# Kernel optimization log

Hardware: AMD Instinct MI355X
Metric: run time of the kernel (lower is better)

The kernel has to match this reference:

```python
import jax, jax.numpy as jnp
import numpy as np

# Dimensions: E experts, T tokens, K hidden, I intermediate (gate+up fused -> 2I)
E, T, K, I = 8, 4096, 2048, 768
TOP_K = 2


def setup_inputs() -> dict:
    key = jax.random.key(0)
    ks = jax.random.split(key, 6)
    hidden_states = jax.random.normal(ks[0], (T, K), dtype=jnp.float32)
    router_logits = jax.random.normal(ks[1], (T, E), dtype=jnp.float32)
    # 2-bit codes {0,1,2} <-> ternary {-1,0,+1} (pack_i2s_weights maps w+1)
    w13_q = jax.random.randint(ks[2], (E, 2 * I, K), 0, 3, dtype=jnp.int32)
    w2_q = jax.random.randint(ks[3], (E, K, I), 0, 3, dtype=jnp.int32)
    # per-input-column alpha scales (always positive, realistic magnitude)
    alpha13 = jax.random.uniform(ks[4], (E, K), dtype=jnp.float32) * 0.04 + 0.01
    alpha2 = jax.random.uniform(ks[5], (E, I), dtype=jnp.float32) * 0.04 + 0.01
    return {
        "hidden_states": hidden_states,
        "router_logits": router_logits,
        "w13_q": w13_q,
        "w2_q": w2_q,
        "alpha13": alpha13,
        "alpha2": alpha2,
    }


def reference(hidden_states, router_logits, w13_q, w2_q, alpha13, alpha2):
    # --- routing: softmax + top-k + renormalize ---
    probs = jax.nn.softmax(router_logits, axis=-1)              # [T, E]
    topk_w, topk_ids = jax.lax.top_k(probs, TOP_K)              # [T, k]
    topk_w = topk_w / jnp.sum(topk_w, axis=-1, keepdims=True)
    # dense combine weights [T, E]; zero for unselected experts
    gates = jnp.sum(
        jax.nn.one_hot(topk_ids, E, dtype=topk_w.dtype) * topk_w[..., None],
        axis=1,
    )

    # --- dequant ternary weights: W = (code - 1) * alpha[input_col] ---
    W13 = (w13_q.astype(jnp.float32) - 1.0) * alpha13[:, None, :]  # [E, 2I, K]
    W2 = (w2_q.astype(jnp.float32) - 1.0) * alpha2[:, None, :]     # [E, K, I]

    # --- grouped expert GEMMs (x @ W^T per expert) ---
    h = jnp.einsum("tk,enk->etn", hidden_states, W13)            # [E, T, 2I]
    g, u = jnp.split(h, 2, axis=-1)
    a = jax.nn.silu(g) * u                                       # [E, T, I]
    y = jnp.einsum("eti,eni->etn", a, W2)                        # [E, T, K]

    # --- combine with routing weights ---
    out = jnp.einsum("te,etk->tk", gates, y)                     # [T, K]
    return out
```

## Files before the change

kernel.cpp:

```cpp
#include <hip/hip_runtime.h>
#include <math.h>

#define E_ 8
#define T_ 4096
#define K_ 2048
#define I_ 768
#define TWOI 1536
#define NPAIR (2*T_)

typedef unsigned short u16;
typedef signed char i8;
typedef __attribute__((ext_vector_type(8))) __bf16 bf16x8;
typedef __attribute__((ext_vector_type(4))) float f32x4;
typedef __attribute__((ext_vector_type(4))) int i32x4;
typedef __attribute__((ext_vector_type(4))) unsigned u32x4;
typedef __attribute__((ext_vector_type(8))) u16 u16x8;
typedef __attribute__((ext_vector_type(4))) u16 u16x4;
typedef __attribute__((ext_vector_type(4))) int int4v;
typedef __attribute__((ext_vector_type(4))) float float4v;

typedef __attribute__((address_space(3))) char lds_c;
typedef __attribute__((address_space(1))) const char g_c;

__device__ inline void gld16(const void* g, void* l) {
    __builtin_amdgcn_global_load_lds((g_c*)g, (lds_c*)l, 16, 0, 0);
}

__device__ inline u16 f2bf(float x) {
    unsigned u = __builtin_bit_cast(unsigned, x);
    unsigned r = 0x7fffu + ((u >> 16) & 1u);
    u += r;
    return (u16)(u >> 16);
}
__device__ inline float bf2f(u16 b) {
    unsigned u = ((unsigned)b) << 16;
    return __builtin_bit_cast(float, u);
}
__device__ inline unsigned pack4(int4v q) {
    return (unsigned)((unsigned char)(char)(q[0] - 1))
         | ((unsigned)((unsigned char)(char)(q[1] - 1)) << 8)
         | ((unsigned)((unsigned char)(char)(q[2] - 1)) << 16)
         | ((unsigned)((unsigned char)(char)(q[3] - 1)) << 24);
}

#define NBLK 2048
__global__ __launch_bounds__(256) void k_fusedA(
    const int* __restrict__ w13q, const int* __restrict__ w2q,
    const float* __restrict__ alpha2, const float* __restrict__ logits,
    const float* __restrict__ x, const float* __restrict__ alpha13,
    i8* __restrict__ wc13, u16* __restrict__ wb2,
    i8* __restrict__ xq, float* __restrict__ sx,
    int* __restrict__ tid2, float* __restrict__ tw, int* __restrict__ cursors)
{
    int tid = threadIdx.x;
    int bid = blockIdx.x;
    if (bid == 0 && tid < E_) cursors[tid] = 0;

    {
        const int4v* src = (const int4v*)w13q;
        unsigned* dst = (unsigned*)wc13;
        const long n = 6291456;
        const long stride = (long)NBLK * 256;
#pragma unroll 2
        for (long u = (long)bid * 256 + tid; u < n; u += stride) {
            int4v q = __builtin_nontemporal_load(src + u);
            dst[u] = pack4(q);
        }
    }
    {
        const int4v* src = (const int4v*)w2q;
        const long n = 3145728;
        const long stride = (long)NBLK * 256;
#pragma unroll 2
        for (long u = (long)bid * 256 + tid; u < n; u += stride) {
            long g = u * 4;
            int i = (int)(g % I_);
            int e = (int)(g / ((long)K_ * I_));
            int4v q = __builtin_nontemporal_load(src + u);
            float4v a = *(const float4v*)(alpha2 + e * I_ + i);
            u16x4 r;
            r[0] = f2bf((float)(q[0] - 1) * a[0]);
            r[1] = f2bf((float)(q[1] - 1) * a[1]);
            r[2] = f2bf((float)(q[2] - 1) * a[2]);
            r[3] = f2bf((float)(q[3] - 1) * a[3]);
            *(u16x4*)(wb2 + g) = r;
        }
    }
    {
        int wv = bid * 4 + (tid >> 6);
        if (wv < T_) {
            int lane = tid & 63;
            int t = wv;
            float l[E_];
#pragma unroll
            for (int e = 0; e < E_; ++e) l[e] = logits[t * E_ + e];
            int e0 = 0; float mx0 = l[0];
#pragma unroll
            for (int e = 1; e < E_; ++e) if (l[e] > mx0) { mx0 = l[e]; e0 = e; }
            int e1 = -1; float mx1 = -1e30f;
#pragma unroll
            for (int e = 0; e < E_; ++e) if (e != e0 && l[e] > mx1) { mx1 = l[e]; e1 = e; }

            float4v xr[8];
#pragma unroll
            for (int c = 0; c < 8; ++c)
                xr[c] = *(const float4v*)(x + (long)t * K_ + c * 256 + lane * 4);

#pragma unroll
            for (int s = 0; s < 2; ++s) {
                int e = s ? e1 : e0;
                int p = 2 * t + s;
                float4v xa[8];
                float m = 0.f;
#pragma unroll
                for (int c = 0; c < 8; ++c) {
                    float4v a = *(const float4v*)(alpha13 + (long)e * K_ + c * 256 + lane * 4);
                    xa[c] = xr[c] * a;
#pragma unroll
                    for (int j = 0; j < 4; ++j) m = fmaxf(m, fabsf(xa[c][j]));
                }
#pragma unroll
                for (int off = 32; off >= 1; off >>= 1) m = fmaxf(m, __shfl_xor(m, off));
                float inv = (m > 0.f) ? 127.0f / m : 0.f;
#pragma unroll
                for (int c = 0; c < 8; ++c) {
                    unsigned pk = 0;
#pragma unroll
                    for (int j = 0; j < 4; ++j) {
                        int qv = __float2int_rn(xa[c][j] * inv);
                        pk |= ((unsigned)(unsigned char)(char)qv) << (8 * j);
                    }
                    *(unsigned*)(xq + (long)p * K_ + c * 256 + lane * 4) = pk;
                }
                if (lane == 0) sx[p] = m / 127.0f;
            }
            if (lane == 0) {
                tid2[2 * t + 0] = e0; tid2[2 * t + 1] = e1;
                float w0 = 1.0f / (1.0f + expf(mx1 - mx0));
                tw[2 * t + 0] = w0; tw[2 * t + 1] = 1.0f - w0;
            }
        }
    }
}

__global__ __launch_bounds__(256) void k_lists2(
    const int* __restrict__ tid2, int* __restrict__ offsets,
    int* __restrict__ cursors, int* __restrict__ pairTok)
{
    int tid = threadIdx.x;
    int c[E_];
#pragma unroll
    for (int e = 0; e < E_; ++e) c[e] = 0;
    for (int j = 0; j < 32; ++j) {
        int v = tid2[tid * 32 + j];
#pragma unroll
        for (int e = 0; e < E_; ++e) c[e] += (v == e) ? 1 : 0;
    }
#pragma unroll
    for (int e = 0; e < E_; ++e)
#pragma unroll
        for (int off = 32; off >= 1; off >>= 1)
            c[e] += __shfl_xor(c[e], off);
    __shared__ int ws[4][E_];
    __shared__ int offs[E_ + 1];
    if ((tid & 63) == 0)
#pragma unroll
        for (int e = 0; e < E_; ++e) ws[tid >> 6][e] = c[e];
    __syncthreads();
    if (tid == 0) {
        int s2 = 0;
        for (int e = 0; e < E_; ++e) {
            int ce = ws[0][e] + ws[1][e] + ws[2][e] + ws[3][e];
            offs[e] = s2; s2 += ce;
        }
        offs[E_] = s2;
        if (blockIdx.x == 0)
            for (int e = 0; e <= E_; ++e) offsets[e] = offs[e];
    }
    __syncthreads();
    int t = blockIdx.x * 256 + tid;
#pragma unroll
    for (int s = 0; s < 2; ++s) {
        int e = tid2[t * 2 + s];
        int pos = atomicAdd(&cursors[e], 1);
        pairTok[offs[e] + pos] = (t << 1) | s;
    }
}

__global__ __launch_bounds__(512, 2) void k_g1i8(
    const i8* __restrict__ A,
    const i8* __restrict__ B,
    const int* __restrict__ pairTok, const int* __restrict__ offsets,
    const float* __restrict__ sx,
    u16* __restrict__ C)
{
    int bid = blockIdx.x;
    int e  = bid & 7;
    int r_ = bid >> 3;
    int mc = r_ / 6;
    int nch = r_ % 6;
    int base = offsets[e];
    int cnt  = offsets[e + 1] - base;
    int m0 = mc * 256;
    if (m0 >= cnt) return;
    int n0 = nch * 128;

    __shared__ __attribute__((aligned(16))) i8 SHM[131072];
    i8* As = SHM;
    i8* Bs = SHM + 65536;

    int tid = threadIdx.x;
    int lane = tid & 63;
    int wid = tid >> 6;
    int wr = wid >> 2, wc = wid & 3;
    int l15 = lane & 15;

    const i8* srcA[4];
    const i8* srcB[4];
#pragma unroll
    for (int j = 0; j < 4; ++j) {
        int chunk = j * 512 + tid;
        int row = chunk >> 3, ch = chunk & 7;
        int colsw = (ch ^ (row & 7)) * 16;
        int ra = m0 + row; if (ra >= cnt) ra = cnt - 1;
        srcA[j] = A + (long)pairTok[base + ra] * K_ + colsw;
        int grow = e * TWOI + (row >> 7) * I_ + n0 + (row & 127);
        srcB[j] = B + (long)grow * K_ + colsw;
    }

    auto stage = [&](int bs, int t) {
        int k0 = t * 128;
        i8* dA = As + bs * 32768;
        i8* dB = Bs + bs * 32768;
#pragma unroll
        for (int j = 0; j < 4; ++j) {
            gld16(srcA[j] + k0, dA + j * 8192 + tid * 16);
            gld16(srcB[j] + k0, dB + j * 8192 + tid * 16);
        }
    };

    int kq16 = ((lane >> 4) & 3) * 16;

    i32x4 a[4][2], b[4][2];
    i32x4 acc[8][4];
#pragma unroll
    for (int mf = 0; mf < 8; ++mf)
#pragma unroll
        for (int nf = 0; nf < 4; ++nf)
            acc[mf][nf] = (i32x4){0, 0, 0, 0};

    auto rdA = [&](int bs, int h64) {
#pragma unroll
        for (int mf = 0; mf < 4; ++mf) {
            int row = wr * 128 + h64 + mf * 16 + l15;
            const i8* p = As + bs * 32768 + row * 128;
            int xr = (row & 7) << 4;
            a[mf][0] = *(const i32x4*)(p + ((kq16) ^ xr));
            a[mf][1] = *(const i32x4*)(p + ((64 + kq16) ^ xr));
        }
    };
    auto rdB = [&](int bs) {
#pragma unroll
        for (int nf = 0; nf < 4; ++nf) {
            int row = wc * 64 + nf * 16 + l15;
            const i8* p = Bs + bs * 32768 + row * 128;
            int xr = (row & 7) << 4;
            b[nf][0] = *(const i32x4*)(p + ((kq16) ^ xr));
            b[nf][1] = *(const i32x4*)(p + ((64 + kq16) ^ xr));
        }
    };
    auto mm = [&](int mh) {
#pragma unroll
        for (int ks = 0; ks < 2; ++ks)
#pragma unroll
            for (int mf = 0; mf < 4; ++mf)
#pragma unroll
                for (int nf = 0; nf < 4; ++nf)
                    acc[mh * 4 + mf][nf] = __builtin_amdgcn_mfma_i32_16x16x64_i8(
                        a[mf][ks], b[nf][ks], acc[mh * 4 + mf][nf], 0, 0, 0);
    };
    auto compute = [&](int bs) {
        rdB(bs);
        rdA(bs, 0);
        mm(0);
        rdA(bs, 64);
        mm(1);
    };

    stage(0, 0);
    __syncthreads();
#pragma unroll 1
    for (int t = 0; t < 16; t += 2) {
        stage(1, t + 1);
        compute(0);
        __syncthreads();
        if (t + 2 < 16) stage(0, t + 2);
        compute(1);
        __syncthreads();
    }

    u16* flat = (u16*)SHM;
#pragma unroll
    for (int mf = 0; mf < 8; ++mf)
#pragma unroll
        for (int nf = 0; nf < 4; ++nf)
#pragma unroll
            for (int rg = 0; rg < 4; ++rg) {
                int row = wr * 128 + mf * 16 + (lane >> 4) * 4 + rg;
                int col = wc * 64 + nf * 16 + l15;
                flat[row * 256 + (col ^ ((row & 7) << 3))] = f2bf((float)acc[mf][nf][rg]);
            }
    __syncthreads();
    int row = tid >> 1;
    if (m0 + row < cnt) {
        float s = sx[pairTok[base + m0 + row]];
        int xr = (row & 7) << 3;
        int half = tid & 1;
        u16* dst = C + (long)(base + m0 + row) * I_ + n0 + half * 64;
#pragma unroll
        for (int jj = 0; jj < 8; ++jj) {
            u16x8 gv = *(const u16x8*)&flat[row * 256 + ((half * 64 + jj * 8) ^ xr)];
            u16x8 uv = *(const u16x8*)&flat[row * 256 + ((128 + half * 64 + jj * 8) ^ xr)];
            u16x8 r;
#pragma unroll
            for (int q = 0; q < 8; ++q) {
                float g = bf2f(gv[q]) * s, u = bf2f(uv[q]) * s;
                r[q] = f2bf(g / (1.0f + expf(-g)) * u);
            }
            *(u16x8*)(dst + jj * 8) = r;
        }
    }
}

__global__ __launch_bounds__(512, 2) void k_g2(
    const u16* __restrict__ A,
    const u16* __restrict__ B,
    const int* __restrict__ pairTok, const int* __restrict__ offsets,
    u16* __restrict__ C)
{
    int bid = blockIdx.x;
    int e  = bid & 7;
    int r_ = bid >> 3;
    int mc = r_ >> 3;
    int nch = r_ & 7;
    int base = offsets[e];
    int cnt  = offsets[e + 1] - base;
    int m0 = mc * 256;
    if (m0 >= cnt) return;
    int n0 = nch * 256;

    __shared__ __attribute__((aligned(16))) char SHM[131072];
    u16* ldsA = (u16*)SHM;
    u16* ldsB = (u16*)(SHM + 65536);

    int tid = threadIdx.x;
    int lane = tid & 63;
    int wid = tid >> 6;
    int wr = wid >> 2, wc = wid & 3;
    int l15 = lane & 15;

    const u16* srcA[2][2];
    const u16* srcB[2][2];
#pragma unroll
    for (int h = 0; h < 2; ++h)
#pragma unroll
        for (int j = 0; j < 2; ++j) {
            int slot = j * 512 + tid;
            int row = slot >> 3, ch = slot & 7;
            int colsw = (ch ^ (row & 7)) * 8;
            int ra = m0 + h * 128 + row;
            if (ra >= cnt) ra = cnt - 1;
            srcA[h][j] = A + (long)(base + ra) * I_ + colsw;
            long brow = (long)e * K_ + n0 + h * 128 + row;
            srcB[h][j] = B + brow * (long)I_ + colsw;
        }
    int d0 = tid * 8, d1 = (512 + tid) * 8;

    auto stage = [&](int bs, int t) {
        int k0 = t * 64;
        u16* dA = ldsA + bs * 16384;
        u16* dB = ldsB + bs * 16384;
#pragma unroll
        for (int h = 0; h < 2; ++h) {
            gld16(srcA[h][0] + k0, dA + h * 8192 + d0);
            gld16(srcA[h][1] + k0, dA + h * 8192 + d1);
            gld16(srcB[h][0] + k0, dB + h * 8192 + d0);
            gld16(srcB[h][1] + k0, dB + h * 8192 + d1);
        }
    };

    int kc0 = ((((lane >> 4) & 3) * 8)) ^ ((lane & 7) * 8);
    int kc1 = (32 + (((lane >> 4) & 3) * 8)) ^ ((lane & 7) * 8);

    bf16x8 a[4][2], b[4][2];
    f32x4 acc[8][4];
#pragma unroll
    for (int mf = 0; mf < 8; ++mf)
#pragma unroll
        for (int nf = 0; nf < 4; ++nf)
            acc[mf][nf] = (f32x4){0.f, 0.f, 0.f, 0.f};

    auto rdA = [&](int bs, int h64) {
#pragma unroll
        for (int mf = 0; mf < 4; ++mf) {
            const u16* p = ldsA + bs * 16384 + (wr * 128 + h64 + mf * 16 + l15) * 64;
            a[mf][0] = __builtin_bit_cast(bf16x8, *(const u16x8*)(p + kc0));
            a[mf][1] = __builtin_bit_cast(bf16x8, *(const u16x8*)(p + kc1));
        }
    };
    auto rdB = [&](int bs) {
#pragma unroll
        for (int nf = 0; nf < 4; ++nf) {
            const u16* p = ldsB + bs * 16384 + (wc * 64 + nf * 16 + l15) * 64;
            b[nf][0] = __builtin_bit_cast(bf16x8, *(const u16x8*)(p + kc0));
            b[nf][1] = __builtin_bit_cast(bf16x8, *(const u16x8*)(p + kc1));
        }
    };
    auto mm = [&](int mh) {
#pragma unroll
        for (int ks = 0; ks < 2; ++ks)
#pragma unroll
            for (int mf = 0; mf < 4; ++mf)
#pragma unroll
                for (int nf = 0; nf < 4; ++nf)
                    acc[mh * 4 + mf][nf] = __builtin_amdgcn_mfma_f32_16x16x32_bf16(
                        a[mf][ks], b[nf][ks], acc[mh * 4 + mf][nf], 0, 0, 0);
    };
    auto compute = [&](int bs) {
        rdB(bs);
        rdA(bs, 0);
        mm(0);
        rdA(bs, 64);
        mm(1);
    };

    stage(0, 0);
    __syncthreads();
#pragma unroll 1
    for (int t = 0; t < 12; t += 2) {
        stage(1, t + 1);
        compute(0);
        __syncthreads();
        if (t + 2 < 12) stage(0, t + 2);
        compute(1);
        __syncthreads();
    }

    u16* flat = (u16*)SHM;
#pragma unroll
    for (int mf = 0; mf < 8; ++mf)
#pragma unroll
        for (int nf = 0; nf < 4; ++nf)
#pragma unroll
            for (int rg = 0; rg < 4; ++rg) {
                int row = wr * 128 + mf * 16 + (lane >> 4) * 4 + rg;
                int col = wc * 64 + nf * 16 + l15;
                flat[row * 256 + (col ^ ((row & 7) << 3))] = f2bf(acc[mf][nf][rg]);
            }
    __syncthreads();
    int row = tid >> 1;
    if (m0 + row < cnt) {
        int xr = (row & 7) << 3;
        int half = tid & 1;
        int pt = pairTok[base + m0 + row];
        u16* dst = C + (long)pt * K_ + n0 + half * 128;
#pragma unroll
        for (int jj = 0; jj < 16; ++jj) {
            *(u16x8*)(dst + jj * 8) =
                *(const u16x8*)&flat[row * 256 + ((half * 128 + jj * 8) ^ xr)];
        }
    }
}

__global__ void k_combine(const u16* __restrict__ yb, const float* __restrict__ tw,
                          float* __restrict__ out) {
    long idx = ((long)blockIdx.x * 256 + threadIdx.x) * 8;
    int t = (int)(idx >> 11);
    float w0 = tw[t * 2 + 0];
    float w1 = tw[t * 2 + 1];
    u16x8 y0 = *(const u16x8*)(yb + (long)(2 * t) * K_ + (idx & (K_ - 1)));
    u16x8 y1 = *(const u16x8*)(yb + (long)(2 * t + 1) * K_ + (idx & (K_ - 1)));
    float4v o0, o1;
#pragma unroll
    for (int j = 0; j < 4; ++j) o0[j] = w0 * bf2f(y0[j]) + w1 * bf2f(y1[j]);
#pragma unroll
    for (int j = 0; j < 4; ++j) o1[j] = w0 * bf2f(y0[4 + j]) + w1 * bf2f(y1[4 + j]);
    *(float4v*)(out + idx) = o0;
    *(float4v*)(out + idx + 4) = o1;
}

extern "C" void kernel_launch(void* const* d_in, const int* in_sizes, int n_in,
                              void* d_out, int out_size, void* d_ws, size_t ws_size,
                              hipStream_t stream) {
    const float* x       = (const float*)d_in[0];
    const float* logits  = (const float*)d_in[1];
    const int*   w13q    = (const int*)d_in[2];
    const int*   w2q     = (const int*)d_in[3];
    const float* alpha13 = (const float*)d_in[4];
    const float* alpha2  = (const float*)d_in[5];
    float* out = (float*)d_out;

    char* ws = (char*)d_ws;
    i8*  wc13 = (i8*)(ws);
    u16* wb2  = (u16*)(ws + 50331648);
    i8*  xq   = (i8*)(ws + 75497472);
    u16* ab   = (u16*)(ws + 92274688);
    u16* yb   = (u16*)(ws + 104857600);
    int* pairTok = (int*)(ws + 138412032);
    int* tid2    = pairTok + NPAIR;
    float* tw    = (float*)(tid2 + NPAIR);
    int* counts  = (int*)(tw + NPAIR);
    int* offsets = counts + 8;
    int* cursors = offsets + 9;
    float* sx    = (float*)(cursors + 8);

    k_fusedA<<<NBLK, 256, 0, stream>>>(
        w13q, w2q, alpha2, logits, x, alpha13, wc13, wb2, xq, sx, tid2, tw, cursors);

    k_lists2<<<T_ / 256, 256, 0, stream>>>(tid2, offsets, cursors, pairTok);

    k_g1i8<<<8 * (T_ / 256) * 6, 512, 0, stream>>>(xq, wc13, pairTok, offsets, sx, ab);

    k_g2<<<8 * (T_ / 256) * (K_ / 256), 512, 0, stream>>>(ab, wb2, pairTok, offsets, yb);

    k_combine<<<((long)T_ * K_) / 8 / 256, 256, 0, stream>>>(yb, tw, out);
}
```

Before: 191.7 us.

## Overlap w2 dequant with GEMM1 and fuse combine into GEMM2 via atomics

Moves the w2 ternary-to-bf16 conversion out of the first prologue kernel into extra blocks appended to the GEMM1 grid, so it runs alongside the int8 GEMM. Fuses the routing-weighted combine into the GEMM2 epilogue using float atomicAdd into the output, which the prologue now zeroes. This drops the bf16 y buffer round-trip and the separate combine launch. The cost is contention from 2-way atomic adds, and the summation order is no longer fixed.

```diff
diff --git a/kernel.cpp b/kernel.cpp
--- a/kernel.cpp
+++ b/kernel.cpp
@@ -45,10 +45,9 @@
 
 #define NBLK 2048
 __global__ __launch_bounds__(256) void k_fusedA(
-    const int* __restrict__ w13q, const int* __restrict__ w2q,
-    const float* __restrict__ alpha2, const float* __restrict__ logits,
+    const int* __restrict__ w13q, const float* __restrict__ logits,
     const float* __restrict__ x, const float* __restrict__ alpha13,
-    i8* __restrict__ wc13, u16* __restrict__ wb2,
+    i8* __restrict__ wc13, float* __restrict__ outz,
     i8* __restrict__ xq, float* __restrict__ sx,
     int* __restrict__ tid2, float* __restrict__ tw, int* __restrict__ cursors)
 {
@@ -56,6 +55,14 @@
     int bid = blockIdx.x;
     if (bid == 0 && tid < E_) cursors[tid] = 0;
 
+    {
+        long u0 = ((long)bid * 256 + tid) * 16;
+        f32x4 z = (f32x4){0.f, 0.f, 0.f, 0.f};
+        *(f32x4*)(outz + u0)      = z;
+        *(f32x4*)(outz + u0 + 4)  = z;
+        *(f32x4*)(outz + u0 + 8)  = z;
+        *(f32x4*)(outz + u0 + 12) = z;
+    }
     {
         const int4v* src = (const int4v*)w13q;
         unsigned* dst = (unsigned*)wc13;
@@ -65,25 +72,6 @@
         for (long u = (long)bid * 256 + tid; u < n; u += stride) {
             int4v q = __builtin_nontemporal_load(src + u);
             dst[u] = pack4(q);
-        }
-    }
-    {
-        const int4v* src = (const int4v*)w2q;
-        const long n = 3145728;
-        const long stride = (long)NBLK * 256;
-#pragma unroll 2
-        for (long u = (long)bid * 256 + tid; u < n; u += stride) {
-            long g = u * 4;
-            int i = (int)(g % I_);
-            int e = (int)(g / ((long)K_ * I_));
-            int4v q = __builtin_nontemporal_load(src + u);
-            float4v a = *(const float4v*)(alpha2 + e * I_ + i);
-            u16x4 r;
-            r[0] = f2bf((float)(q[0] - 1) * a[0]);
-            r[1] = f2bf((float)(q[1] - 1) * a[1]);
-            r[2] = f2bf((float)(q[2] - 1) * a[2]);
-            r[3] = f2bf((float)(q[3] - 1) * a[3]);
-            *(u16x4*)(wb2 + g) = r;
         }
     }
     {
@@ -187,14 +175,39 @@
     }
 }
 
+#define G1GRID (8 * (T_ / 256) * 6)
+#define CVT2BLK 256
 __global__ __launch_bounds__(512, 2) void k_g1i8(
     const i8* __restrict__ A,
     const i8* __restrict__ B,
     const int* __restrict__ pairTok, const int* __restrict__ offsets,
     const float* __restrict__ sx,
-    u16* __restrict__ C)
+    u16* __restrict__ C,
+    const int* __restrict__ w2q, const float* __restrict__ alpha2,
+    u16* __restrict__ wb2)
 {
     int bid = blockIdx.x;
+    if (bid >= G1GRID) {
+        int cb = bid - G1GRID;
+        const int4v* src = (const int4v*)w2q;
+        const long n = 3145728;
+        const long stride = (long)CVT2BLK * 512;
+        for (long u = (long)cb * 512 + threadIdx.x; u < n; u += stride) {
+            long g = u * 4;
+            int i = (int)(g % I_);
+            int e = (int)(g / ((long)K_ * I_));
+            int4v q = __builtin_nontemporal_load(src + u);
+            float4v a = *(const float4v*)(alpha2 + e * I_ + i);
+            u16x4 r;
+            r[0] = f2bf((float)(q[0] - 1) * a[0]);
+            r[1] = f2bf((float)(q[1] - 1) * a[1]);
+            r[2] = f2bf((float)(q[2] - 1) * a[2]);
+            r[3] = f2bf((float)(q[3] - 1) * a[3]);
+            *(u16x4*)(wb2 + g) = r;
+        }
+        return;
+    }
+
     int e  = bid & 7;
     int r_ = bid >> 3;
     int mc = r_ / 6;
@@ -336,7 +349,8 @@
     const u16* __restrict__ A,
     const u16* __restrict__ B,
     const int* __restrict__ pairTok, const int* __restrict__ offsets,
-    u16* __restrict__ C)
+    const float* __restrict__ tw,
+    float* __restrict__ out)
 {
     int bid = blockIdx.x;
     int e  = bid & 7;
@@ -350,6 +364,8 @@
     int n0 = nch * 256;
 
     __shared__ __attribute__((aligned(16))) char SHM[131072];
+    __shared__ float rowW[256];
+    __shared__ int   rowT[256];
     u16* ldsA = (u16*)SHM;
     u16* ldsB = (u16*)(SHM + 65536);
 
@@ -457,36 +473,28 @@
                 int col = wc * 64 + nf * 16 + l15;
                 flat[row * 256 + (col ^ ((row & 7) << 3))] = f2bf(acc[mf][nf][rg]);
             }
+    if (tid < 256) {
+        int row = tid;
+        if (m0 + row < cnt) {
+            int pt = pairTok[base + m0 + row];
+            rowW[row] = tw[pt];
+            rowT[row] = pt >> 1;
+        } else {
+            rowW[row] = 0.f;
+            rowT[row] = -1;
+        }
+    }
     __syncthreads();
-    int row = tid >> 1;
-    if (m0 + row < cnt) {
-        int xr = (row & 7) << 3;
-        int half = tid & 1;
-        int pt = pairTok[base + m0 + row];
-        u16* dst = C + (long)pt * K_ + n0 + half * 128;
-#pragma unroll
-        for (int jj = 0; jj < 16; ++jj) {
-            *(u16x8*)(dst + jj * 8) =
-                *(const u16x8*)&flat[row * 256 + ((half * 128 + jj * 8) ^ xr)];
-        }
-    }
-}
-
-__global__ void k_combine(const u16* __restrict__ yb, const float* __restrict__ tw,
-                          float* __restrict__ out) {
-    long idx = ((long)blockIdx.x * 256 + threadIdx.x) * 8;
-    int t = (int)(idx >> 11);
-    float w0 = tw[t * 2 + 0];
-    float w1 = tw[t * 2 + 1];
-    u16x8 y0 = *(const u16x8*)(yb + (long)(2 * t) * K_ + (idx & (K_ - 1)));
-    u16x8 y1 = *(const u16x8*)(yb + (long)(2 * t + 1) * K_ + (idx & (K_ - 1)));
-    float4v o0, o1;
-#pragma unroll
-    for (int j = 0; j < 4; ++j) o0[j] = w0 * bf2f(y0[j]) + w1 * bf2f(y1[j]);
-#pragma unroll
-    for (int j = 0; j < 4; ++j) o1[j] = w0 * bf2f(y0[4 + j]) + w1 * bf2f(y1[4 + j]);
-    *(float4v*)(out + idx) = o0;
-    *(float4v*)(out + idx + 4) = o1;
+    int nvalid = cnt - m0; if (nvalid > 256) nvalid = 256;
+#pragma unroll 4
+    for (int j = 0; j < 128; ++j) {
+        int idx = j * 512 + tid;
+        int row = idx >> 8;
+        if (row >= nvalid) break;
+        int col = idx & 255;
+        float v = bf2f(flat[row * 256 + (col ^ ((row & 7) << 3))]) * rowW[row];
+        atomicAdd(&out[(long)rowT[row] * K_ + n0 + col], v);
+    }
 }
 
 extern "C" void kernel_launch(void* const* d_in, const int* in_sizes, int n_in,
@@ -505,7 +513,6 @@
     u16* wb2  = (u16*)(ws + 50331648);
     i8*  xq   = (i8*)(ws + 75497472);
     u16* ab   = (u16*)(ws + 92274688);
-    u16* yb   = (u16*)(ws + 104857600);
     int* pairTok = (int*)(ws + 138412032);
     int* tid2    = pairTok + NPAIR;
     float* tw    = (float*)(tid2 + NPAIR);
@@ -515,13 +522,12 @@
     float* sx    = (float*)(cursors + 8);
 
     k_fusedA<<<NBLK, 256, 0, stream>>>(
-        w13q, w2q, alpha2, logits, x, alpha13, wc13, wb2, xq, sx, tid2, tw, cursors);
+        w13q, logits, x, alpha13, wc13, out, xq, sx, tid2, tw, cursors);
 
     k_lists2<<<T_ / 256, 256, 0, stream>>>(tid2, offsets, cursors, pairTok);
 
-    k_g1i8<<<8 * (T_ / 256) * 6, 512, 0, stream>>>(xq, wc13, pairTok, offsets, sx, ab);
-
-    k_g2<<<8 * (T_ / 256) * (K_ / 256), 512, 0, stream>>>(ab, wb2, pairTok, offsets, yb);
-
-    k_combine<<<((long)T_ * K_) / 8 / 256, 256, 0, stream>>>(yb, tw, out);
-}
+    k_g1i8<<<G1GRID + CVT2BLK, 512, 0, stream>>>(
+        xq, wc13, pairTok, offsets, sx, ab, w2q, alpha2, wb2);
+
+    k_g2<<<8 * (T_ / 256) * (K_ / 256), 512, 0, stream>>>(ab, wb2, pairTok, offsets, tw, out);
+}
```

After: 233.6 us. +21.8%, slower.

## Fold routing list construction into front kernel with redundant per-block routing

Applied to the files above, without the earlier changes.

Removes the separate list-building kernel by adding 16 extra blocks to the front kernel. Each of these blocks recomputes top-2 routing for all tokens into shared memory, counts experts, derives global offsets and a per-block prefix, then writes its slice of pairTok with shared-memory atomics instead of global cursors. This drops one kernel launch and the tid2 round trip through global memory. In exchange it adds redundant routing work, 24KB+ of shared memory per block in the front kernel (which may cut occupancy for the bulk weight-conversion blocks), and order within each expert is no longer deterministic.

```diff
diff --git a/kernel.cpp b/kernel.cpp
--- a/kernel.cpp
+++ b/kernel.cpp
@@ -10,10 +10,10 @@
 
 typedef unsigned short u16;
 typedef signed char i8;
+typedef unsigned char u8;
 typedef __attribute__((ext_vector_type(8))) __bf16 bf16x8;
 typedef __attribute__((ext_vector_type(4))) float f32x4;
 typedef __attribute__((ext_vector_type(4))) int i32x4;
-typedef __attribute__((ext_vector_type(4))) unsigned u32x4;
 typedef __attribute__((ext_vector_type(8))) u16 u16x8;
 typedef __attribute__((ext_vector_type(4))) u16 u16x4;
 typedef __attribute__((ext_vector_type(4))) int int4v;
@@ -43,26 +43,104 @@
          | ((unsigned)((unsigned char)(char)(q[3] - 1)) << 24);
 }
 
+__device__ inline void route2(const float* l, int& e0, int& e1, float& mx0, float& mx1) {
+    e0 = 0; mx0 = l[0];
+#pragma unroll
+    for (int e = 1; e < E_; ++e) if (l[e] > mx0) { mx0 = l[e]; e0 = e; }
+    e1 = -1; mx1 = -1e30f;
+#pragma unroll
+    for (int e = 0; e < E_; ++e) if (e != e0 && l[e] > mx1) { mx1 = l[e]; e1 = e; }
+}
+
 #define NBLK 2048
-__global__ __launch_bounds__(256) void k_fusedA(
+#define LISTB 16
+__global__ __launch_bounds__(256) void k_front(
     const int* __restrict__ w13q, const int* __restrict__ w2q,
     const float* __restrict__ alpha2, const float* __restrict__ logits,
     const float* __restrict__ x, const float* __restrict__ alpha13,
     i8* __restrict__ wc13, u16* __restrict__ wb2,
     i8* __restrict__ xq, float* __restrict__ sx,
-    int* __restrict__ tid2, float* __restrict__ tw, int* __restrict__ cursors)
+    float* __restrict__ tw, int* __restrict__ offsets, int* __restrict__ pairTok)
 {
+    __shared__ u8 eArr[NPAIR];
+    __shared__ int cmat[256][E_];
+    __shared__ int offsS[E_ + 1];
+    __shared__ int preS[E_];
+    __shared__ int curS[E_];
+
     int tid = threadIdx.x;
     int bid = blockIdx.x;
-    if (bid == 0 && tid < E_) cursors[tid] = 0;
-
+
+    if (bid < LISTB) {
+        int b = bid;
+#pragma unroll 1
+        for (int it = 0; it < 16; ++it) {
+            int t = tid + 256 * it;
+            float l[E_];
+#pragma unroll
+            for (int e = 0; e < E_; ++e) l[e] = logits[t * E_ + e];
+            int e0, e1; float mx0, mx1;
+            route2(l, e0, e1, mx0, mx1);
+            eArr[2 * t + 0] = (u8)e0;
+            eArr[2 * t + 1] = (u8)e1;
+            if ((t >> 8) == b) {
+                float w0 = 1.0f / (1.0f + expf(mx1 - mx0));
+                tw[2 * t + 0] = w0; tw[2 * t + 1] = 1.0f - w0;
+            }
+        }
+        __syncthreads();
+        int c[E_];
+#pragma unroll
+        for (int e = 0; e < E_; ++e) c[e] = 0;
+#pragma unroll 1
+        for (int j = 0; j < 32; ++j) {
+            int v = eArr[tid * 32 + j];
+#pragma unroll
+            for (int e = 0; e < E_; ++e) c[e] += (v == e) ? 1 : 0;
+        }
+#pragma unroll
+        for (int e = 0; e < E_; ++e) cmat[tid][e] = c[e];
+        __syncthreads();
+        if (tid < E_) {
+            int e = tid;
+            int tot = 0, pre = 0;
+            int lim = b * 16;
+            for (int j = 0; j < 256; ++j) {
+                int v = cmat[j][e];
+                tot += v;
+                if (j < lim) pre += v;
+            }
+            cmat[0][e] = tot;
+            preS[e] = pre;
+            curS[e] = 0;
+        }
+        __syncthreads();
+        if (tid == 0) {
+            int s2 = 0;
+            for (int e = 0; e < E_; ++e) { offsS[e] = s2; s2 += cmat[0][e]; }
+            offsS[E_] = s2;
+            if (b == 0)
+                for (int e = 0; e <= E_; ++e) offsets[e] = offsS[e];
+        }
+        __syncthreads();
+        int t = b * 256 + tid;
+#pragma unroll
+        for (int s = 0; s < 2; ++s) {
+            int e = eArr[2 * t + s];
+            int pos = atomicAdd(&curS[e], 1);
+            pairTok[offsS[e] + preS[e] + pos] = (t << 1) | s;
+        }
+        return;
+    }
+
+    int sid = bid - LISTB;
     {
         const int4v* src = (const int4v*)w13q;
         unsigned* dst = (unsigned*)wc13;
         const long n = 6291456;
         const long stride = (long)NBLK * 256;
 #pragma unroll 2
-        for (long u = (long)bid * 256 + tid; u < n; u += stride) {
+        for (long u = (long)sid * 256 + tid; u < n; u += stride) {
             int4v q = __builtin_nontemporal_load(src + u);
             dst[u] = pack4(q);
         }
@@ -72,7 +150,7 @@
         const long n = 3145728;
         const long stride = (long)NBLK * 256;
 #pragma unroll 2
-        for (long u = (long)bid * 256 + tid; u < n; u += stride) {
+        for (long u = (long)sid * 256 + tid; u < n; u += stride) {
             long g = u * 4;
             int i = (int)(g % I_);
             int e = (int)(g / ((long)K_ * I_));
@@ -87,19 +165,15 @@
         }
     }
     {
-        int wv = bid * 4 + (tid >> 6);
+        int wv = sid * 4 + (tid >> 6);
         if (wv < T_) {
             int lane = tid & 63;
             int t = wv;
             float l[E_];
 #pragma unroll
             for (int e = 0; e < E_; ++e) l[e] = logits[t * E_ + e];
-            int e0 = 0; float mx0 = l[0];
-#pragma unroll
-            for (int e = 1; e < E_; ++e) if (l[e] > mx0) { mx0 = l[e]; e0 = e; }
-            int e1 = -1; float mx1 = -1e30f;
-#pragma unroll
-            for (int e = 0; e < E_; ++e) if (e != e0 && l[e] > mx1) { mx1 = l[e]; e1 = e; }
+            int e0, e1; float mx0, mx1;
+            route2(l, e0, e1, mx0, mx1);
 
             float4v xr[8];
 #pragma unroll
@@ -134,56 +208,7 @@
                 }
                 if (lane == 0) sx[p] = m / 127.0f;
             }
-            if (lane == 0) {
-                tid2[2 * t + 0] = e0; tid2[2 * t + 1] = e1;
-                float w0 = 1.0f / (1.0f + expf(mx1 - mx0));
-                tw[2 * t + 0] = w0; tw[2 * t + 1] = 1.0f - w0;
-            }
-        }
-    }
-}
-
-__global__ __launch_bounds__(256) void k_lists2(
-    const int* __restrict__ tid2, int* __restrict__ offsets,
-    int* __restrict__ cursors, int* __restrict__ pairTok)
-{
-    int tid = threadIdx.x;
-    int c[E_];
-#pragma unroll
-    for (int e = 0; e < E_; ++e) c[e] = 0;
-    for (int j = 0; j < 32; ++j) {
-        int v = tid2[tid * 32 + j];
-#pragma unroll
-        for (int e = 0; e < E_; ++e) c[e] += (v == e) ? 1 : 0;
-    }
-#pragma unroll
-    for (int e = 0; e < E_; ++e)
-#pragma unroll
-        for (int off = 32; off >= 1; off >>= 1)
-            c[e] += __shfl_xor(c[e], off);
-    __shared__ int ws[4][E_];
-    __shared__ int offs[E_ + 1];
-    if ((tid & 63) == 0)
-#pragma unroll
-        for (int e = 0; e < E_; ++e) ws[tid >> 6][e] = c[e];
-    __syncthreads();
-    if (tid == 0) {
-        int s2 = 0;
-        for (int e = 0; e < E_; ++e) {
-            int ce = ws[0][e] + ws[1][e] + ws[2][e] + ws[3][e];
-            offs[e] = s2; s2 += ce;
-        }
-        offs[E_] = s2;
-        if (blockIdx.x == 0)
-            for (int e = 0; e <= E_; ++e) offsets[e] = offs[e];
-    }
-    __syncthreads();
-    int t = blockIdx.x * 256 + tid;
-#pragma unroll
-    for (int s = 0; s < 2; ++s) {
-        int e = tid2[t * 2 + s];
-        int pos = atomicAdd(&cursors[e], 1);
-        pairTok[offs[e] + pos] = (t << 1) | s;
+        }
     }
 }
 
@@ -514,10 +539,8 @@
     int* cursors = offsets + 9;
     float* sx    = (float*)(cursors + 8);
 
-    k_fusedA<<<NBLK, 256, 0, stream>>>(
-        w13q, w2q, alpha2, logits, x, alpha13, wc13, wb2, xq, sx, tid2, tw, cursors);
-
-    k_lists2<<<T_ / 256, 256, 0, stream>>>(tid2, offsets, cursors, pairTok);
+    k_front<<<LISTB + NBLK, 256, 0, stream>>>(
+        w13q, w2q, alpha2, logits, x, alpha13, wc13, wb2, xq, sx, tw, offsets, pairTok);
 
     k_g1i8<<<8 * (T_ / 256) * 6, 512, 0, stream>>>(xq, wc13, pairTok, offsets, sx, ab);
 
```

New measurement: 155.7 us. 1.23x faster.
